# Performance work log

Hardware: AMD Instinct MI355X
Metric: run time of the kernel (lower is better)

The kernel has to match this reference:

```python
import jax, jax.numpy as jnp
import numpy as np

T, H, I, E, TOP_K = 4096, 2048, 768, 16, 2


def _pack_i2s(tern):
    # tern: int8 in {-1,0,1}, shape [..., K] with K % 4 == 0
    m = (tern + 1).astype(jnp.uint8)  # map to {0,1,2}
    m = m.reshape(*tern.shape[:-1], -1, 4)
    return (m[..., 0] | (m[..., 1] << 2) | (m[..., 2] << 4) | (m[..., 3] << 6)).astype(jnp.uint8)


def _quantize_alpha(alpha):
    # per-column alpha -> int8 with global scale (quantize_alpha_int8)
    scale = jnp.maximum(jnp.abs(alpha).max(), 1e-8) / 127.0
    q = jnp.clip(jnp.round(alpha / scale), -128, 127).astype(jnp.int8)
    return q, scale.astype(jnp.float32)


def _unpack_i2s(packed, K, alpha):
    # packed: uint8 [..., N, K//4]; alpha: [..., K] per input column
    shifts = jnp.array([0, 2, 4, 6], dtype=jnp.uint8)
    ext = (packed[..., None] >> shifts) & jnp.uint8(3)  # [..., N, K//4, 4]
    vals = ext.reshape(*packed.shape[:-1], K).astype(jnp.float32) - 1.0  # {-1,0,1}
    return vals * alpha[..., None, :]


def setup_inputs() -> dict:
    key = jax.random.key(0)
    ks = jax.random.split(key, 6)
    x = jax.random.normal(ks[0], (T, H), dtype=jnp.float32)
    router_logits = jax.random.normal(ks[1], (T, E), dtype=jnp.float32)
    tern13 = jax.random.randint(ks[2], (E, 2 * I, H), -1, 2, dtype=jnp.int8)
    tern2 = jax.random.randint(ks[3], (E, H, I), -1, 2, dtype=jnp.int8)
    a13 = jax.random.uniform(ks[4], (E, H), minval=0.01, maxval=0.05, dtype=jnp.float32)
    a2 = jax.random.uniform(ks[5], (E, I), minval=0.01, maxval=0.05, dtype=jnp.float32)
    w13_alpha_q, w13_alpha_scale = _quantize_alpha(a13)
    w2_alpha_q, w2_alpha_scale = _quantize_alpha(a2)
    return {
        "x": x,
        "router_logits": router_logits,
        "w13_packed": _pack_i2s(tern13),
        "w13_alpha_q": w13_alpha_q,
        "w13_alpha_scale": w13_alpha_scale,
        "w2_packed": _pack_i2s(tern2),
        "w2_alpha_q": w2_alpha_q,
        "w2_alpha_scale": w2_alpha_scale,
    }


def reference(x, router_logits, w13_packed, w13_alpha_q, w13_alpha_scale,
              w2_packed, w2_alpha_q, w2_alpha_scale):
    # dequant int8 alphas, then dequant 2-bit ternary weights
    a13 = w13_alpha_q.astype(jnp.float32) * w13_alpha_scale  # [E, H]
    a2 = w2_alpha_q.astype(jnp.float32) * w2_alpha_scale     # [E, I]
    w13 = _unpack_i2s(w13_packed, H, a13)  # [E, 2I, H]
    w2 = _unpack_i2s(w2_packed, I, a2)     # [E, H, I]

    # top-k routing with renormalized softmax weights
    probs = jax.nn.softmax(router_logits, axis=-1)
    topw, topi = jax.lax.top_k(probs, TOP_K)           # [T, k]
    topw = topw / topw.sum(axis=-1, keepdims=True)
    combine = jnp.sum(jax.nn.one_hot(topi, E, dtype=x.dtype) * topw[..., None], axis=1)  # [T, E]

    # grouped expert matmuls (dense dispatch over experts)
    gu = jnp.einsum('th,enh->ten', x, w13)             # [T, E, 2I]
    gate, up = jnp.split(gu, 2, axis=-1)
    act = jax.nn.silu(gate) * up                       # [T, E, I]
    down = jnp.einsum('tei,ehi->teh', act, w2)         # [T, E, H]
    return jnp.einsum('te,teh->th', combine, down)     # [T, H]
```

## Files before the change

### kernel.cpp

```cpp
#include <hip/hip_runtime.h>
#include <stdint.h>

#define T_TOK 4096
#define HDIM  2048
#define IDIM  768
#define NEXP  16
#define NPAIR (T_TOK * 2)
#define PAIR_CAP (NPAIR + 256)

typedef float f32x4 __attribute__((ext_vector_type(4)));
typedef __bf16 bf16x8 __attribute__((ext_vector_type(8)));
typedef unsigned short u16x8 __attribute__((ext_vector_type(8)));
typedef unsigned int u32;
typedef u32 u32x4 __attribute__((ext_vector_type(4)));
typedef const __attribute__((address_space(1))) u32* as1_u32p;
typedef __attribute__((address_space(3))) u32* as3_u32p;

__device__ __forceinline__ unsigned short f2bf(float f) {
  u32 u = __float_as_uint(f);
  u += 0x7FFFu + ((u >> 16) & 1u);
  return (unsigned short)(u >> 16);
}

__device__ __forceinline__ f32x4 mfma16(bf16x8 a, bf16x8 b, f32x4 c) {
  return __builtin_amdgcn_mfma_f32_16x16x32_bf16(a, b, c, 0, 0, 0);
}

__device__ __forceinline__ bf16x8 expand8(u32 w, int qshift) {
  w >>= qshift;
  const u32 t0 = w & 0x03030303u;
  const u32 h0 = __builtin_amdgcn_perm(0u, 0x003F00BFu, t0);
  const u32 l0 = __builtin_amdgcn_perm(0u, 0x00800080u, t0);
  const u32 t1 = (w >> 2) & 0x03030303u;
  const u32 h1 = __builtin_amdgcn_perm(0u, 0x003F00BFu, t1);
  const u32 l1 = __builtin_amdgcn_perm(0u, 0x00800080u, t1);
  u32x4 o;
  o[0] = __builtin_amdgcn_perm(h0, l0, 0x05010400u);
  o[1] = __builtin_amdgcn_perm(h0, l0, 0x07030602u);
  o[2] = __builtin_amdgcn_perm(h1, l1, 0x05010400u);
  o[3] = __builtin_amdgcn_perm(h1, l1, 0x07030602u);
  return __builtin_bit_cast(bf16x8, o);
}

__global__ __launch_bounds__(256) void route_kernel(
    const float* __restrict__ logits, int* __restrict__ counts,
    int* __restrict__ t2i, float* __restrict__ t2w) {
  const int t = blockIdx.x * 256 + threadIdx.x;
  if (t >= T_TOK) return;
  const float* l = logits + t * NEXP;
  float m0 = -1e30f, m1 = -1e30f;
  int i0 = 0, i1 = 0;
#pragma unroll
  for (int j = 0; j < NEXP; ++j) {
    const float v = l[j];
    if (v > m0) { m1 = m0; i1 = i0; m0 = v; i0 = j; }
    else if (v > m1) { m1 = v; i1 = j; }
  }
  const float w0 = 1.0f / (1.0f + expf(m1 - m0));
  t2i[t] = i0 | (i1 << 8);
  t2w[t] = w0;
  atomicAdd(&counts[i0], 1);
  atomicAdd(&counts[i1], 1);
}

__global__ void scan_kernel(const int* __restrict__ counts,
                            int* __restrict__ offs, int* __restrict__ cursor) {
  if (threadIdx.x == 0) {
    int s = 0;
    for (int e = 0; e < NEXP; ++e) { offs[e] = s; cursor[e] = s; s += counts[e]; }
    offs[NEXP] = s;
  }
}

__global__ __launch_bounds__(256) void fill_kernel(
    const int* __restrict__ t2i, const float* __restrict__ t2w,
    int* __restrict__ cursor, int* __restrict__ pair_token,
    float* __restrict__ pair_wt, int* __restrict__ pair_eid,
    int* __restrict__ t2p0, int* __restrict__ t2p1) {
  const int t = blockIdx.x * 256 + threadIdx.x;
  if (t >= T_TOK) return;
  const int ii = t2i[t];
  const float w0 = t2w[t];
  const int i0 = ii & 255, i1 = (ii >> 8) & 255;
  const int p0 = atomicAdd(&cursor[i0], 1);
  pair_token[p0] = t; pair_wt[p0] = w0; pair_eid[p0] = i0;
  const int p1 = atomicAdd(&cursor[i1], 1);
  pair_token[p1] = t; pair_wt[p1] = 1.0f - w0; pair_eid[p1] = i1;
  t2p0[t] = p0; t2p1[t] = p1;
}

__global__ __launch_bounds__(256) void repack_kernel(
    const int* __restrict__ w, u32* __restrict__ o) {
  const int j0 = (blockIdx.x * 256 + threadIdx.x) * 4;
  const int4* w4 = (const int4*)w;
  uint4 r;
#pragma unroll
  for (int k = 0; k < 4; ++k) {
    const int4 a = w4[j0 + k];
    u32 x = (u32)(a.x & 255) | ((u32)(a.y & 255) << 8) |
            ((u32)(a.z & 255) << 16) | ((u32)(a.w & 255) << 24);
    u32 t = (x ^ (x >> 12)) & 0x0000F0F0u; x ^= t ^ (t << 12);
    t = (x ^ (x >> 6)) & 0x00CC00CCu;      x ^= t ^ (t << 6);
    ((u32*)&r)[k] = x;
  }
  ((uint4*)o)[blockIdx.x * 256 + threadIdx.x] = r;
}

__global__ __launch_bounds__(256) void xg_kernel(
    const float* __restrict__ x, const int* __restrict__ a13q,
    const float* __restrict__ s13p, const int* __restrict__ pair_token,
    const int* __restrict__ pair_eid, unsigned short* __restrict__ xg) {
  const int p = blockIdx.x;
  const int t = pair_token[p];
  const int e = pair_eid[p];
  const float s13 = *s13p;
  const int h0 = threadIdx.x * 8;
  const float* xp = x + (size_t)t * HDIM + h0;
  const int* ap = a13q + (size_t)e * HDIM + h0;
  const float4 x0 = ((const float4*)xp)[0];
  const float4 x1 = ((const float4*)xp)[1];
  const int4 a0 = ((const int4*)ap)[0];
  const int4 a1 = ((const int4*)ap)[1];
  u16x8 q;
  q[0] = f2bf(x0.x * (float)a0.x * s13);
  q[1] = f2bf(x0.y * (float)a0.y * s13);
  q[2] = f2bf(x0.z * (float)a0.z * s13);
  q[3] = f2bf(x0.w * (float)a0.w * s13);
  q[4] = f2bf(x1.x * (float)a1.x * s13);
  q[5] = f2bf(x1.y * (float)a1.y * s13);
  q[6] = f2bf(x1.z * (float)a1.z * s13);
  q[7] = f2bf(x1.w * (float)a1.w * s13);
  *(u16x8*)(xg + (size_t)p * HDIM + h0) = q;
}

#define DMA_A(src, pitch, dst0, dst1, sidx)                                          \
  {                                                                                  \
    _Pragma("unroll") for (int c = 0; c < 2; ++c) {                                  \
      const unsigned short* gp =                                                     \
          src + (arow0 + wave * 32 + c * 16 + arow) * (pitch) + (sidx) * 64 + acol;  \
      unsigned short* lp = dst0 + (wave * 32 + c * 16) * 32;                         \
      __builtin_amdgcn_global_load_lds((as1_u32p)(const void*)gp,                    \
                                       (as3_u32p)(void*)lp, 16, 0, 0);               \
    }                                                                                \
    _Pragma("unroll") for (int c = 0; c < 2; ++c) {                                  \
      const unsigned short* gp =                                                     \
          src + (arow0 + wave * 32 + c * 16 + arow) * (pitch) + (sidx) * 64 + 32 +   \
          acol;                                                                      \
      unsigned short* lp = dst1 + (wave * 32 + c * 16) * 32;                         \
      __builtin_amdgcn_global_load_lds((as1_u32p)(const void*)gp,                    \
                                       (as3_u32p)(void*)lp, 16, 0, 0);               \
    }                                                                                \
  }

#define DMA_B1(dstq, sidx)                                                           \
  if (wave < 2) {                                                                    \
    const u32* gq = wq13 + ((size_t)e * (2 * IDIM) + wave * IDIM + nT * 64 + lane) * \
                               (HDIM / 16) + (size_t)(sidx) * 4;                     \
    u32* lp = (dstq) + wave * 256;                                                   \
    __builtin_amdgcn_global_load_lds((as1_u32p)(const void*)gq,                      \
                                     (as3_u32p)(void*)lp, 16, 0, 0);                 \
  }

#define DMA_B2(dstq, sidx)                                                           \
  if (wave < 2) {                                                                    \
    const u32* gq = wq2 + ((size_t)e * HDIM + nT * 128 + wave * 64 + lane) *         \
                              (IDIM / 16) + (size_t)(sidx) * 4;                      \
    u32* lp = (dstq) + wave * 256;                                                   \
    __builtin_amdgcn_global_load_lds((as1_u32p)(const void*)gq,                      \
                                     (as3_u32p)(void*)lp, 16, 0, 0);                 \
  }

#define G1_HALF(sAp, sBp, h)                                                        \
  {                                                                                 \
    bf16x8 af[4];                                                                   \
    _Pragma("unroll") for (int mi = 0; mi < 4; ++mi)                                \
        af[mi] = *(const bf16x8*)((sAp) + (wm * 64 + mi * 16 + ln) * 32 + quad * 8);\
    const u32 c0 = (sBp)[(wn * 32 + ln) * 4 + 2 * (h) + qsel];                      \
    const u32 c1 = (sBp)[(wn * 32 + 16 + ln) * 4 + 2 * (h) + qsel];                 \
    const u32 c2 = (sBp)[(64 + wn * 32 + ln) * 4 + 2 * (h) + qsel];                 \
    const u32 c3 = (sBp)[(64 + wn * 32 + 16 + ln) * 4 + 2 * (h) + qsel];            \
    const bf16x8 b0 = expand8(c0, qshift), b1 = expand8(c1, qshift);                \
    const bf16x8 b2 = expand8(c2, qshift), b3 = expand8(c3, qshift);                \
    _Pragma("unroll") for (int mi = 0; mi < 4; ++mi) {                              \
      acc[mi][0] = mfma16(af[mi], b0, acc[mi][0]);                                  \
      acc[mi][1] = mfma16(af[mi], b1, acc[mi][1]);                                  \
      acc[mi][2] = mfma16(af[mi], b2, acc[mi][2]);                                  \
      acc[mi][3] = mfma16(af[mi], b3, acc[mi][3]);                                  \
    }                                                                               \
  }

#define G2_HALF(sAp, sBp, h)                                                        \
  {                                                                                 \
    bf16x8 af[4];                                                                   \
    _Pragma("unroll") for (int mi = 0; mi < 4; ++mi)                                \
        af[mi] = *(const bf16x8*)((sAp) + (wm * 64 + mi * 16 + ln) * 32 + quad * 8);\
    const u32 c0 = (sBp)[(wn * 64 + ln) * 4 + 2 * (h) + qsel];                      \
    const u32 c1 = (sBp)[(wn * 64 + 16 + ln) * 4 + 2 * (h) + qsel];                 \
    const u32 c2 = (sBp)[(wn * 64 + 32 + ln) * 4 + 2 * (h) + qsel];                 \
    const u32 c3 = (sBp)[(wn * 64 + 48 + ln) * 4 + 2 * (h) + qsel];                 \
    const bf16x8 b0 = expand8(c0, qshift), b1 = expand8(c1, qshift);                \
    const bf16x8 b2 = expand8(c2, qshift), b3 = expand8(c3, qshift);                \
    _Pragma("unroll") for (int mi = 0; mi < 4; ++mi) {                              \
      acc[mi][0] = mfma16(af[mi], b0, acc[mi][0]);                                  \
      acc[mi][1] = mfma16(af[mi], b1, acc[mi][1]);                                  \
      acc[mi][2] = mfma16(af[mi], b2, acc[mi][2]);                                  \
      acc[mi][3] = mfma16(af[mi], b3, acc[mi][3]);                                  \
    }                                                                               \
  }

__global__ __launch_bounds__(256, 4) void gemm1_kernel(
    const u32* __restrict__ wq13, const int* __restrict__ a2q,
    const float* __restrict__ s2p, const int* __restrict__ counts,
    const int* __restrict__ offs, const float* __restrict__ pair_wt,
    const unsigned short* __restrict__ xg, unsigned short* __restrict__ act) {
  const int id = blockIdx.x;
  const int xcd = id & 7, sblk = id >> 3;
  const int nT = sblk % 12;
  const int gg = (sblk / 12) * 8 + xcd;
  const int e = gg & 15, mT = gg >> 4;
  const int cnt = counts[e];
  if (mT * 128 >= cnt) return;
  const int base = offs[e];
  const int tid = threadIdx.x;

  __shared__ __align__(16) unsigned short sA[2][2][128 * 32];
  __shared__ __align__(16) u32 sBq[2][512];

  const int wave = tid >> 6, lane = tid & 63;
  const int wm = wave >> 1, wn = wave & 1;
  const int quad = lane >> 4, ln = lane & 15;
  const int qsel = quad >> 1;
  const int qshift = (quad & 1) * 4;

  const int arow = lane >> 2;
  const int acol = (lane & 3) * 8;
  const size_t arow0 = (size_t)(base + mT * 128);

  f32x4 acc[4][4] = {};

  DMA_A(xg, HDIM, sA[0][0], sA[0][1], 0);
  DMA_B1(sBq[0], 0);

  const int NT = HDIM / 64;
  for (int j2 = 0; j2 < NT / 2; ++j2) {
    const int j = 2 * j2;
    __syncthreads();
    DMA_A(xg, HDIM, sA[1][0], sA[1][1], j + 1);
    DMA_B1(sBq[1], j + 1);
    __builtin_amdgcn_s_setprio(1);
    G1_HALF(sA[0][0], sBq[0], 0);
    G1_HALF(sA[0][1], sBq[0], 1);
    __builtin_amdgcn_s_setprio(0);
    __syncthreads();
    if (j2 + 1 < NT / 2) {
      DMA_A(xg, HDIM, sA[0][0], sA[0][1], j + 2);
      DMA_B1(sBq[0], j + 2);
    }
    __builtin_amdgcn_s_setprio(1);
    G1_HALF(sA[1][0], sBq[1], 0);
    G1_HALF(sA[1][1], sBq[1], 1);
    __builtin_amdgcn_s_setprio(0);
  }

  const float s2v = *s2p;
#pragma unroll
  for (int gi = 0; gi < 2; ++gi) {
    const int i = nT * 64 + wn * 32 + gi * 16 + ln;
    const float a2v = (float)a2q[e * IDIM + i] * s2v;
#pragma unroll
    for (int mi = 0; mi < 4; ++mi) {
      const f32x4 g = acc[mi][gi];
      const f32x4 u = acc[mi][gi + 2];
#pragma unroll
      for (int r = 0; r < 4; ++r) {
        const int m = mT * 128 + wm * 64 + mi * 16 + quad * 4 + r;
        if (m < cnt) {
          const float wt = pair_wt[base + m];
          const float gv = g[r];
          const float av = gv / (1.0f + __expf(-gv)) * u[r] * a2v * wt;
          act[(size_t)(base + m) * IDIM + i] = f2bf(av);
        }
      }
    }
  }
}

__global__ __launch_bounds__(256, 4) void gemm2_kernel(
    const u32* __restrict__ wq2, const int* __restrict__ counts,
    const int* __restrict__ offs, const unsigned short* __restrict__ act,
    unsigned short* __restrict__ down) {
  const int id = blockIdx.x;
  const int xcd = id & 7, sblk = id >> 3;
  const int nT = sblk & 15;
  const int gg = (sblk >> 4) * 8 + xcd;
  const int e = gg & 15, mT = gg >> 4;
  const int cnt = counts[e];
  if (mT * 128 >= cnt) return;
  const int base = offs[e];
  const int tid = threadIdx.x;

  __shared__ __align__(16) unsigned short sA[2][2][128 * 32];
  __shared__ __align__(16) u32 sBq[2][512];

  const int wave = tid >> 6, lane = tid & 63;
  const int wm = wave >> 1, wn = wave & 1;
  const int quad = lane >> 4, ln = lane & 15;
  const int qsel = quad >> 1;
  const int qshift = (quad & 1) * 4;

  const int arow = lane >> 2;
  const int acol = (lane & 3) * 8;
  const size_t arow0 = (size_t)(base + mT * 128);

  f32x4 acc[4][4] = {};

  DMA_A(act, IDIM, sA[0][0], sA[0][1], 0);
  DMA_B2(sBq[0], 0);

  const int NT = IDIM / 64;
  for (int j2 = 0; j2 < NT / 2; ++j2) {
    const int j = 2 * j2;
    __syncthreads();
    DMA_A(act, IDIM, sA[1][0], sA[1][1], j + 1);
    DMA_B2(sBq[1], j + 1);
    __builtin_amdgcn_s_setprio(1);
    G2_HALF(sA[0][0], sBq[0], 0);
    G2_HALF(sA[0][1], sBq[0], 1);
    __builtin_amdgcn_s_setprio(0);
    __syncthreads();
    if (j2 + 1 < NT / 2) {
      DMA_A(act, IDIM, sA[0][0], sA[0][1], j + 2);
      DMA_B2(sBq[0], j + 2);
    }
    __builtin_amdgcn_s_setprio(1);
    G2_HALF(sA[1][0], sBq[1], 0);
    G2_HALF(sA[1][1], sBq[1], 1);
    __builtin_amdgcn_s_setprio(0);
  }

#pragma unroll
  for (int mi = 0; mi < 4; ++mi) {
#pragma unroll
    for (int r = 0; r < 4; ++r) {
      const int ml = wm * 64 + mi * 16 + quad * 4 + r;
      const int m = mT * 128 + ml;
      if (m < cnt) {
        unsigned short* drow = down + (size_t)(base + m) * HDIM + nT * 128 + wn * 64;
#pragma unroll
        for (int ni = 0; ni < 4; ++ni)
          drow[ni * 16 + ln] = f2bf(acc[mi][ni][r]);
      }
    }
  }
}

__global__ __launch_bounds__(256) void combine_kernel(
    const int* __restrict__ t2p0, const int* __restrict__ t2p1,
    const unsigned short* __restrict__ down, float* __restrict__ out) {
  const int t = blockIdx.x;
  const int h = threadIdx.x * 8;
  const u16x8 a = *(const u16x8*)(down + (size_t)t2p0[t] * HDIM + h);
  const u16x8 b = *(const u16x8*)(down + (size_t)t2p1[t] * HDIM + h);
  f32x4 o0, o1;
#pragma unroll
  for (int j = 0; j < 4; ++j) {
    o0[j] = __uint_as_float((u32)a[j] << 16) + __uint_as_float((u32)b[j] << 16);
    o1[j] = __uint_as_float((u32)a[j + 4] << 16) + __uint_as_float((u32)b[j + 4] << 16);
  }
  float* o = out + (size_t)t * HDIM + h;
  *(f32x4*)(o) = o0;
  *(f32x4*)(o + 4) = o1;
}

extern "C" void kernel_launch(void* const* d_in, const int* in_sizes, int n_in,
                              void* d_out, int out_size, void* d_ws, size_t ws_size,
                              hipStream_t stream) {
  const float* x      = (const float*)d_in[0];
  const float* logits = (const float*)d_in[1];
  const int*   w13p   = (const int*)d_in[2];
  const int*   a13q   = (const int*)d_in[3];
  const float* s13    = (const float*)d_in[4];
  const int*   w2p    = (const int*)d_in[5];
  const int*   a2q    = (const int*)d_in[6];
  const float* s2     = (const float*)d_in[7];
  float* out = (float*)d_out;

  char* ws = (char*)d_ws;
  int*   counts     = (int*)(ws + 0);
  int*   cursor     = (int*)(ws + 64);
  int*   offs       = (int*)(ws + 128);
  int*   t2i        = (int*)(ws + 256);
  float* t2w        = (float*)(ws + 256 + 4 * T_TOK);
  int*   t2p0       = (int*)(ws + 256 + 8 * T_TOK);
  int*   t2p1       = (int*)(ws + 256 + 12 * T_TOK);
  int*   pair_token = (int*)(ws + 256 + 16 * T_TOK);
  float* pair_wt    = (float*)(ws + 256 + 16 * T_TOK + 4 * PAIR_CAP);
  int*   pair_eid   = (int*)(ws + 256 + 16 * T_TOK + 8 * PAIR_CAP);
  const size_t hdr_end = ((size_t)(256 + 16 * T_TOK + 12 * PAIR_CAP) + 255) & ~(size_t)255;

  const size_t n32_13 = (size_t)NEXP * 2 * IDIM * (HDIM / 16);
  const size_t n32_2  = (size_t)NEXP * HDIM * (IDIM / 16);
  const size_t rp13_b = n32_13 * 4, rp2_b = n32_2 * 4;
  const size_t xg_b   = (size_t)PAIR_CAP * HDIM * 2;

  u32* rp13 = (u32*)(ws + hdr_end);
  u32* rp2  = (u32*)(ws + hdr_end + rp13_b);
  unsigned short* xg  = (unsigned short*)(ws + hdr_end + rp13_b + rp2_b);
  unsigned short* act = (unsigned short*)(ws + hdr_end + rp13_b + rp2_b + xg_b);
  unsigned short* down = xg;

  hipMemsetAsync(counts, 0, 256, stream);
  route_kernel<<<T_TOK / 256, 256, 0, stream>>>(logits, counts, t2i, t2w);
  scan_kernel<<<1, 64, 0, stream>>>(counts, offs, cursor);
  fill_kernel<<<T_TOK / 256, 256, 0, stream>>>(t2i, t2w, cursor, pair_token, pair_wt,
                                               pair_eid, t2p0, t2p1);
  repack_kernel<<<(int)(n32_13 / 1024), 256, 0, stream>>>(w13p, rp13);
  repack_kernel<<<(int)(n32_2 / 1024), 256, 0, stream>>>(w2p, rp2);
  xg_kernel<<<NPAIR, 256, 0, stream>>>(x, a13q, s13, pair_token, pair_eid, xg);

  gemm1_kernel<<<6144, 256, 0, stream>>>(rp13, a2q, s2, counts, offs, pair_wt, xg, act);
  gemm2_kernel<<<8192, 256, 0, stream>>>(rp2, counts, offs, act, down);
  combine_kernel<<<T_TOK, 256, 0, stream>>>(t2p0, t2p1, down, out);
}
```

Before: 331.5 us.

## Fuse combine into gemm2 epilogue via atomics; merge scan into fill and repack launches

```diff
diff --git a/kernel.cpp b/kernel.cpp
--- a/kernel.cpp
+++ b/kernel.cpp
@@ -63,35 +63,48 @@
   atomicAdd(&counts[i1], 1);
 }
 
-__global__ void scan_kernel(const int* __restrict__ counts,
-                            int* __restrict__ offs, int* __restrict__ cursor) {
-  if (threadIdx.x == 0) {
-    int s = 0;
-    for (int e = 0; e < NEXP; ++e) { offs[e] = s; cursor[e] = s; s += counts[e]; }
-    offs[NEXP] = s;
-  }
-}
-
 __global__ __launch_bounds__(256) void fill_kernel(
-    const int* __restrict__ t2i, const float* __restrict__ t2w,
-    int* __restrict__ cursor, int* __restrict__ pair_token,
-    float* __restrict__ pair_wt, int* __restrict__ pair_eid,
-    int* __restrict__ t2p0, int* __restrict__ t2p1) {
+    const int* __restrict__ counts, const int* __restrict__ t2i,
+    const float* __restrict__ t2w, int* __restrict__ cursor,
+    int* __restrict__ offs, int* __restrict__ pair_token,
+    float* __restrict__ pair_wt, int* __restrict__ pair_eid) {
   const int t = blockIdx.x * 256 + threadIdx.x;
   if (t >= T_TOK) return;
   const int ii = t2i[t];
+  const int i0 = ii & 255, i1 = (ii >> 8) & 255;
+  int o0 = 0, o1 = 0, s = 0;
+#pragma unroll
+  for (int j = 0; j < NEXP; ++j) {
+    const int c = counts[j];
+    o0 += (j < i0) ? c : 0;
+    o1 += (j < i1) ? c : 0;
+    s += c;
+  }
+  if (t == 0) {
+    int run = 0;
+#pragma unroll
+    for (int j = 0; j < NEXP; ++j) { offs[j] = run; run += counts[j]; }
+    offs[NEXP] = run;
+  }
   const float w0 = t2w[t];
-  const int i0 = ii & 255, i1 = (ii >> 8) & 255;
-  const int p0 = atomicAdd(&cursor[i0], 1);
+  const int p0 = o0 + atomicAdd(&cursor[i0], 1);
   pair_token[p0] = t; pair_wt[p0] = w0; pair_eid[p0] = i0;
-  const int p1 = atomicAdd(&cursor[i1], 1);
+  const int p1 = o1 + atomicAdd(&cursor[i1], 1);
   pair_token[p1] = t; pair_wt[p1] = 1.0f - w0; pair_eid[p1] = i1;
-  t2p0[t] = p0; t2p1[t] = p1;
-}
-
+}
+
+#define RP13_BLOCKS 3072
+#define RP2_BLOCKS  1536
 __global__ __launch_bounds__(256) void repack_kernel(
-    const int* __restrict__ w, u32* __restrict__ o) {
-  const int j0 = (blockIdx.x * 256 + threadIdx.x) * 4;
+    const int* __restrict__ w13, u32* __restrict__ o13,
+    const int* __restrict__ w2, u32* __restrict__ o2) {
+  const int gid = blockIdx.x;
+  const int* w;
+  u32* o;
+  int b;
+  if (gid < RP13_BLOCKS) { w = w13; o = o13; b = gid; }
+  else                   { w = w2;  o = o2;  b = gid - RP13_BLOCKS; }
+  const int j0 = (b * 256 + threadIdx.x) * 4;
   const int4* w4 = (const int4*)w;
   uint4 r;
 #pragma unroll
@@ -103,7 +116,7 @@
     t = (x ^ (x >> 6)) & 0x00CC00CCu;      x ^= t ^ (t << 6);
     ((u32*)&r)[k] = x;
   }
-  ((uint4*)o)[blockIdx.x * 256 + threadIdx.x] = r;
+  ((uint4*)o)[b * 256 + threadIdx.x] = r;
 }
 
 __global__ __launch_bounds__(256) void xg_kernel(
@@ -287,8 +300,8 @@
 
 __global__ __launch_bounds__(256, 4) void gemm2_kernel(
     const u32* __restrict__ wq2, const int* __restrict__ counts,
-    const int* __restrict__ offs, const unsigned short* __restrict__ act,
-    unsigned short* __restrict__ down) {
+    const int* __restrict__ offs, const int* __restrict__ pair_token,
+    const unsigned short* __restrict__ act, float* __restrict__ out) {
   const int id = blockIdx.x;
   const int xcd = id & 7, sblk = id >> 3;
   const int nT = sblk & 15;
@@ -345,31 +358,14 @@
       const int ml = wm * 64 + mi * 16 + quad * 4 + r;
       const int m = mT * 128 + ml;
       if (m < cnt) {
-        unsigned short* drow = down + (size_t)(base + m) * HDIM + nT * 128 + wn * 64;
+        const int tok = pair_token[base + m];
+        float* orow = out + (size_t)tok * HDIM + nT * 128 + wn * 64;
 #pragma unroll
         for (int ni = 0; ni < 4; ++ni)
-          drow[ni * 16 + ln] = f2bf(acc[mi][ni][r]);
+          atomicAdd(&orow[ni * 16 + ln], acc[mi][ni][r]);
       }
     }
   }
-}
-
-__global__ __launch_bounds__(256) void combine_kernel(
-    const int* __restrict__ t2p0, const int* __restrict__ t2p1,
-    const unsigned short* __restrict__ down, float* __restrict__ out) {
-  const int t = blockIdx.x;
-  const int h = threadIdx.x * 8;
-  const u16x8 a = *(const u16x8*)(down + (size_t)t2p0[t] * HDIM + h);
-  const u16x8 b = *(const u16x8*)(down + (size_t)t2p1[t] * HDIM + h);
-  f32x4 o0, o1;
-#pragma unroll
-  for (int j = 0; j < 4; ++j) {
-    o0[j] = __uint_as_float((u32)a[j] << 16) + __uint_as_float((u32)b[j] << 16);
-    o1[j] = __uint_as_float((u32)a[j + 4] << 16) + __uint_as_float((u32)b[j + 4] << 16);
-  }
-  float* o = out + (size_t)t * HDIM + h;
-  *(f32x4*)(o) = o0;
-  *(f32x4*)(o + 4) = o1;
 }
 
 extern "C" void kernel_launch(void* const* d_in, const int* in_sizes, int n_in,
@@ -391,8 +387,6 @@
   int*   offs       = (int*)(ws + 128);
   int*   t2i        = (int*)(ws + 256);
   float* t2w        = (float*)(ws + 256 + 4 * T_TOK);
-  int*   t2p0       = (int*)(ws + 256 + 8 * T_TOK);
-  int*   t2p1       = (int*)(ws + 256 + 12 * T_TOK);
   int*   pair_token = (int*)(ws + 256 + 16 * T_TOK);
   float* pair_wt    = (float*)(ws + 256 + 16 * T_TOK + 4 * PAIR_CAP);
   int*   pair_eid   = (int*)(ws + 256 + 16 * T_TOK + 8 * PAIR_CAP);
@@ -407,18 +401,15 @@
   u32* rp2  = (u32*)(ws + hdr_end + rp13_b);
   unsigned short* xg  = (unsigned short*)(ws + hdr_end + rp13_b + rp2_b);
   unsigned short* act = (unsigned short*)(ws + hdr_end + rp13_b + rp2_b + xg_b);
-  unsigned short* down = xg;
 
   hipMemsetAsync(counts, 0, 256, stream);
+  hipMemsetAsync(out, 0, (size_t)T_TOK * HDIM * 4, stream);
   route_kernel<<<T_TOK / 256, 256, 0, stream>>>(logits, counts, t2i, t2w);
-  scan_kernel<<<1, 64, 0, stream>>>(counts, offs, cursor);
-  fill_kernel<<<T_TOK / 256, 256, 0, stream>>>(t2i, t2w, cursor, pair_token, pair_wt,
-                                               pair_eid, t2p0, t2p1);
-  repack_kernel<<<(int)(n32_13 / 1024), 256, 0, stream>>>(w13p, rp13);
-  repack_kernel<<<(int)(n32_2 / 1024), 256, 0, stream>>>(w2p, rp2);
+  fill_kernel<<<T_TOK / 256, 256, 0, stream>>>(counts, t2i, t2w, cursor, offs,
+                                               pair_token, pair_wt, pair_eid);
+  repack_kernel<<<RP13_BLOCKS + RP2_BLOCKS, 256, 0, stream>>>(w13p, rp13, w2p, rp2);
   xg_kernel<<<NPAIR, 256, 0, stream>>>(x, a13q, s13, pair_token, pair_eid, xg);
 
   gemm1_kernel<<<6144, 256, 0, stream>>>(rp13, a2q, s2, counts, offs, pair_wt, xg, act);
-  gemm2_kernel<<<8192, 256, 0, stream>>>(rp2, counts, offs, act, down);
-  combine_kernel<<<T_TOK, 256, 0, stream>>>(t2p0, t2p1, down, out);
-}
+  gemm2_kernel<<<8192, 256, 0, stream>>>(rp2, counts, offs, pair_token, act, out);
+}
```

New measurement: 357.9 us. 1.08x slower.
